# Kernel tuning notes

Hardware: AMD Instinct MI355X
Metric: run time of the kernel (lower is better)

## Reference

```python
import jax, jax.numpy as jnp
import numpy as np

K, D = 1024, 256


def setup_inputs() -> dict:
    key = jax.random.key(0)
    k1, k2 = jax.random.split(key)
    z_e = jax.random.normal(k1, (32, D, 32, 32), dtype=jnp.float32)
    # torch init: uniform_(-1/K, 1/K)
    emb_weight = jax.random.uniform(k2, (K, D), minval=-1.0 / K, maxval=1.0 / K, dtype=jnp.float32)
    return {"z_e": z_e, "emb_weight": emb_weight}


def reference(z_e, emb_weight):
    B, C, W, H = z_e.shape
    # [B, W, H, C] -> flatten to [N, C]
    z = jnp.transpose(z_e, (0, 2, 3, 1))
    z_flat = z.reshape(-1, C)
    # squared euclidean distances; argmin is identical to argmin of cdist
    d2 = (
        jnp.sum(z_flat * z_flat, axis=1, keepdims=True)
        - 2.0 * (z_flat @ emb_weight.T)
        + jnp.sum(emb_weight * emb_weight, axis=1)
    )  # [N, K]
    indices = jnp.argmin(d2, axis=1)  # [N]
    z_q = emb_weight[indices].reshape(B, W, H, C)
    # straight-through: forward value equals z_q, gradient passes to z_e
    z_q_st = z + jax.lax.stop_gradient(z_q - z)
    z_q_out = jnp.transpose(z_q, (0, 3, 1, 2))
    z_q_st_out = jnp.transpose(z_q_st, (0, 3, 1, 2))
    return (z_q_st_out, z_q_out, indices.reshape(B, W * H))
```

## Files before the change

### kernel.cpp

```cpp
#include <hip/hip_runtime.h>
#include <cfloat>
#include <cstdint>

#define THRESH 1.25e-4f

typedef __attribute__((ext_vector_type(8))) _Float16 half8;
typedef __attribute__((ext_vector_type(8))) unsigned short upk8;
typedef __attribute__((ext_vector_type(4))) float facc4;

__device__ __forceinline__ unsigned short f2h(float x) {
  _Float16 h = (_Float16)x;
  return __builtin_bit_cast(unsigned short, h);
}


__global__ __launch_bounds__(256) void precompute_kernel(
    const float* __restrict__ emb, float* __restrict__ Csq,
    unsigned short* __restrict__ ehT, int* __restrict__ flagCount) {
  int blk = blockIdx.x, t = threadIdx.x;
  if (blk < 4) {
    int k = blk * 256 + t;
    const float4* e4 = (const float4*)(emb + ((size_t)k << 8));
    double acc = 0.0;
    for (int d4 = 0; d4 < 64; ++d4) {
      float4 e = e4[d4];
      acc += (double)(e.x * e.x) + (double)(e.y * e.y) +
             (double)(e.z * e.z) + (double)(e.w * e.w);
    }
    Csq[k] = (float)acc;
    if (blk == 0 && t == 0) *flagCount = 0;
  } else {
    int linear = (blk - 4) * 256 + t;
    int code = linear & 1023, kg = linear >> 10;
    const float* ep = emb + ((size_t)code << 8) + (kg << 3);
    float4 e0 = *(const float4*)ep;
    float4 e1 = *(const float4*)(ep + 4);
    upk8 pk;
    pk[0] = f2h(e0.x); pk[1] = f2h(e0.y); pk[2] = f2h(e0.z); pk[3] = f2h(e0.w);
    pk[4] = f2h(e1.x); pk[5] = f2h(e1.y); pk[6] = f2h(e1.z); pk[7] = f2h(e1.w);
    *(upk8*)(ehT + ((size_t)linear << 3)) = pk;
  }
}

__device__ __forceinline__ void stage_slab(
    const unsigned short* __restrict__ ehT, char* slab, int s, int t) {
  int w6 = t & 0x1C0;
#pragma unroll
  for (int i = 0; i < 16; ++i) {
    int slot = (i << 9) + t;
    int kg = slot >> 8, cl = slot & 255;
    const unsigned short* g = ehT + (((size_t)(kg << 10) + (s << 8) + cl) << 3);
    char* lp = slab + (((i << 9) + w6) << 4);
    __builtin_amdgcn_global_load_lds(
        (const __attribute__((address_space(1))) unsigned int*)g,
        (__attribute__((address_space(3))) unsigned int*)lp, 16, 0, 0);
  }
}

__global__ __launch_bounds__(512, 2) void phase1_kernel(
    const float* __restrict__ z, const unsigned short* __restrict__ ehT,
    const float* __restrict__ Csq, float* __restrict__ A,
    int* __restrict__ idxbuf, int* __restrict__ flagCount,
    int* __restrict__ flagList) {
  __shared__ char slab[131072] __attribute__((aligned(16)));
  __shared__ float Cs[1024];
  __shared__ float mm1[2][4][32], mm2[2][4][32];
  __shared__ int mbi[2][4][32];

  int t = threadIdx.x;
  int n0 = blockIdx.x << 7;
  int b = n0 >> 10, wh0 = n0 & 1023;
  int w = t >> 6, l = t & 63;
  int wv = w & 3, wn = w >> 2;
  int lx = l & 15, lg = l >> 4;

  stage_slab(ehT, slab, 0, t);
  ((float2*)Cs)[t] = ((const float2*)Csq)[t];

  half8 afr[2][8];
  double nacc[2] = {0.0, 0.0};
  const float* zb = z + (((size_t)(b * 256)) << 10) + wh0 + wv * 32 + lx;
#pragma unroll
  for (int mi = 0; mi < 2; ++mi) {
#pragma unroll
    for (int kk = 0; kk < 8; ++kk) {
      upk8 pk;
#pragma unroll
      for (int j = 0; j < 8; ++j) {
        int c = kk * 32 + lg * 8 + j;
        float x = zb[((size_t)c << 10) + mi * 16];
        nacc[mi] += (double)(x * x);
        pk[j] = f2h(-2.0f * x);
      }
      afr[mi][kk] = __builtin_bit_cast(half8, pk);
    }
  }
#pragma unroll
  for (int mi = 0; mi < 2; ++mi) {
    double s = nacc[mi];
    s += __shfl_xor(s, 16);
    s += __shfl_xor(s, 32);
    if (wn == 0 && lg == 0) A[n0 + wv * 32 + mi * 16 + lx] = (float)s;
  }
  __syncthreads();

  float m1[8], m2[8];
  int bi[8];
#pragma unroll
  for (int s8 = 0; s8 < 8; ++s8) { m1[s8] = FLT_MAX; m2[s8] = FLT_MAX; bi[s8] = 0; }

  for (int s = 0; s < 4; ++s) {
    facc4 acc[2][8];
#pragma unroll
    for (int mi = 0; mi < 2; ++mi)
#pragma unroll
      for (int nj = 0; nj < 8; ++nj) {
        facc4 zf = {0.0f, 0.0f, 0.0f, 0.0f};
        acc[mi][nj] = zf;
      }
#pragma unroll
    for (int kk = 0; kk < 8; ++kk) {
      const char* base = slab + ((((kk << 2) + lg) << 8) + (wn << 7) + lx) * 16;
#pragma unroll
      for (int nj = 0; nj < 8; ++nj) {
        half8 bv = *(const half8*)(base + (nj << 8));
        acc[0][nj] = __builtin_amdgcn_mfma_f32_16x16x32_f16(afr[0][kk], bv, acc[0][nj], 0, 0, 0);
        acc[1][nj] = __builtin_amdgcn_mfma_f32_16x16x32_f16(afr[1][kk], bv, acc[1][nj], 0, 0, 0);
      }
    }
    int cbase = s * 256 + wn * 128;
#pragma unroll
    for (int nj = 0; nj < 8; ++nj) {
      float csv = Cs[cbase + nj * 16 + lx];
      int code = cbase + nj * 16 + lx;
#pragma unroll
      for (int mi = 0; mi < 2; ++mi)
#pragma unroll
        for (int reg = 0; reg < 4; ++reg) {
          int s8 = mi * 4 + reg;
          float sv = acc[mi][nj][reg] + csv;
          float hi = fmaxf(sv, m1[s8]);
          bool lt = sv < m1[s8];
          m1[s8] = lt ? sv : m1[s8];
          bi[s8] = lt ? code : bi[s8];
          m2[s8] = fminf(m2[s8], hi);
        }
    }
    __syncthreads();
    if (s < 3) {
      stage_slab(ehT, slab, s + 1, t);
      __syncthreads();
    }
  }

#pragma unroll
  for (int s8 = 0; s8 < 8; ++s8) {
    float M1 = m1[s8], M2 = m2[s8];
    int BI = bi[s8];
    for (int off = 8; off > 0; off >>= 1) {
      float om1 = __shfl_xor(M1, off, 16);
      float om2 = __shfl_xor(M2, off, 16);
      int obi = __shfl_xor(BI, off, 16);
      float lo = fminf(M2, om2);
      bool take = (om1 < M1) || (om1 == M1 && obi < BI);
      float loser = take ? M1 : om1;
      M2 = fminf(lo, loser);
      if (take) { M1 = om1; BI = obi; }
    }
    if (lx == 0) {
      int row = ((s8 >> 2) << 4) + (lg << 2) + (s8 & 3);
      mm1[wn][wv][row] = M1; mm2[wn][wv][row] = M2; mbi[wn][wv][row] = BI;
    }
  }
  __syncthreads();
  if (wn == 0 && lx == 0) {
#pragma unroll
    for (int s8 = 0; s8 < 8; ++s8) {
      int row = ((s8 >> 2) << 4) + (lg << 2) + (s8 & 3);
      float a1v = mm1[0][wv][row], a2v = mm2[0][wv][row];
      int ab = mbi[0][wv][row];
      float b1v = mm1[1][wv][row], b2v = mm2[1][wv][row];
      int bb = mbi[1][wv][row];
      bool tb = (b1v < a1v) || (b1v == a1v && bb < ab);
      float M1 = tb ? b1v : a1v;
      int BI = tb ? bb : ab;
      float M2 = fminf(fminf(a2v, b2v), tb ? a1v : b1v);
      int n = n0 + wv * 32 + row;
      idxbuf[n] = BI;
      if (M2 - M1 < THRESH) {
        int pos = atomicAdd(flagCount, 1);
        flagList[pos] = n;
      }
    }
  }
}

__global__ __launch_bounds__(256) void phase2_kernel(
    const float* __restrict__ z, const float* __restrict__ emb,
    const float* __restrict__ Csq, const float* __restrict__ A,
    int* __restrict__ idxbuf, const int* __restrict__ flagCount,
    const int* __restrict__ flagList) {
  __shared__ float zq[4][260];
  __shared__ float Anv[4];
  __shared__ int nn[4];
  __shared__ float sq[4][4];
  __shared__ int sk[4][4];
  int t = threadIdx.x;
  int w = t >> 6, l = t & 63;
  int cnt = *flagCount;
  int nit = (cnt + 3) >> 2;
  for (int it = blockIdx.x; it < nit; it += gridDim.x) {
    __syncthreads();
    int base = it << 2;
    int mcnt = min(4, cnt - base);
    if (t < 4) {
      if (t < mcnt) { int n = flagList[base + t]; nn[t] = n; Anv[t] = A[n]; }
      else nn[t] = -1;
    }
    __syncthreads();
#pragma unroll
    for (int v = 0; v < 4; ++v) {
      int n = nn[v];
      if (n >= 0) {
        int bb = n >> 10, wh = n & 1023;
        zq[v][t] = z[(((size_t)(bb * 256 + t)) << 10) + wh];
      }
    }
    __syncthreads();

    float dot[4][4];
#pragma unroll
    for (int r = 0; r < 4; ++r)
#pragma unroll
      for (int v = 0; v < 4; ++v) dot[r][v] = 0.0f;

    const float4* e0 = (const float4*)(emb + ((size_t)(t + 0) << 8));
    const float4* e1 = (const float4*)(emb + ((size_t)(t + 256) << 8));
    const float4* e2 = (const float4*)(emb + ((size_t)(t + 512) << 8));
    const float4* e3 = (const float4*)(emb + ((size_t)(t + 768) << 8));
#pragma unroll 8
    for (int d4 = 0; d4 < 64; ++d4) {
      float4 ea = e0[d4], eb = e1[d4], ec = e2[d4], ed = e3[d4];
#pragma unroll
      for (int v = 0; v < 4; ++v) {
        float4 zv = *(const float4*)&zq[v][d4 * 4];
        dot[0][v] += zv.x * ea.x + zv.y * ea.y + zv.z * ea.z + zv.w * ea.w;
        dot[1][v] += zv.x * eb.x + zv.y * eb.y + zv.z * eb.z + zv.w * eb.w;
        dot[2][v] += zv.x * ec.x + zv.y * ec.y + zv.z * ec.z + zv.w * ec.w;
        dot[3][v] += zv.x * ed.x + zv.y * ed.y + zv.z * ed.z + zv.w * ed.w;
      }
    }

    float bq[4];
    int bk[4];
#pragma unroll
    for (int v = 0; v < 4; ++v) { bq[v] = FLT_MAX; bk[v] = 0; }
#pragma unroll
    for (int r = 0; r < 4; ++r) {
      int k = t + (r << 8);
      float Ck = Csq[k];
#pragma unroll
      for (int v = 0; v < 4; ++v) {
        float qv = (Anv[v] - 2.0f * dot[r][v]) + Ck;
        if (qv < bq[v]) { bq[v] = qv; bk[v] = k; }
      }
    }

#pragma unroll
    for (int v = 0; v < 4; ++v) {
      float q = bq[v];
      int kk = bk[v];
      for (int off = 32; off > 0; off >>= 1) {
        float oq = __shfl_xor(q, off);
        int ok = __shfl_xor(kk, off);
        if (oq < q || (oq == q && ok < kk)) { q = oq; kk = ok; }
      }
      if (l == 0) { sq[v][w] = q; sk[v][w] = kk; }
    }
    __syncthreads();
    if (t < mcnt) {
      float q = sq[t][0];
      int kk = sk[t][0];
#pragma unroll
      for (int j = 1; j < 4; ++j) {
        float oq = sq[t][j];
        int ok = sk[t][j];
        if (oq < q || (oq == q && ok < kk)) { q = oq; kk = ok; }
      }
      idxbuf[nn[t]] = kk;
    }
  }
}

__global__ __launch_bounds__(256) void gather_kernel(
    const float* __restrict__ emb, const int* __restrict__ idxbuf,
    float* __restrict__ out) {
  __shared__ int sidx[32];
  __shared__ float se[256][34];
  int tid = threadIdx.x;
  int blk = blockIdx.x;
  int n0 = blk * 32;
  int b = n0 >> 10, wh0 = n0 & 1023;
  float* out0 = out;
  float* out1 = out + 8388608;
  float* out2 = out + 16777216;
  if (tid < 32) {
    int ix = idxbuf[n0 + tid];
    sidx[tid] = ix;
    out2[n0 + tid] = (float)ix;
  }
  __syncthreads();
  {
    int v = tid >> 3, d8 = tid & 7;
    int row = sidx[v];
    const float4* e4 = (const float4*)(emb + ((size_t)row << 8));
    for (int it = 0; it < 8; ++it) {
      int d4 = it * 8 + d8;
      float4 e = e4[d4];
      se[d4 * 4 + 0][v] = e.x; se[d4 * 4 + 1][v] = e.y;
      se[d4 * 4 + 2][v] = e.z; se[d4 * 4 + 3][v] = e.w;
    }
  }
  __syncthreads();
  {
    int v = tid & 31, cg = tid >> 5;
    for (int c = cg; c < 256; c += 8) {
      float val = se[c][v];
      size_t o = (((size_t)(b * 256 + c)) << 10) + wh0 + v;
      out0[o] = val;
      out1[o] = val;
    }
  }
}

extern "C" void kernel_launch(void* const* d_in, const int* in_sizes, int n_in,
                              void* d_out, int out_size, void* d_ws, size_t ws_size,
                              hipStream_t stream) {
  const float* z = (const float*)d_in[0];
  const float* emb = (const float*)d_in[1];
  float* ws = (float*)d_ws;
  float* Csq = ws;
  float* A = ws + 1024;
  int* idxbuf = (int*)(ws + 33792);
  int* flagCount = (int*)(ws + 66560);
  int* flagList = (int*)(ws + 66576);
  unsigned short* ehT = (unsigned short*)(ws + 99344);

  precompute_kernel<<<132, 256, 0, stream>>>(emb, Csq, ehT, flagCount);
  phase1_kernel<<<256, 512, 0, stream>>>(z, ehT, Csq, A, idxbuf, flagCount, flagList);
  phase2_kernel<<<1024, 256, 0, stream>>>(z, emb, Csq, A, idxbuf, flagCount, flagList);
  gather_kernel<<<1024, 256, 0, stream>>>(emb, idxbuf, (float*)d_out);
}
```

Before: 102.3 us.

## Double-buffer codebook LDS staging to overlap global loads with MFMA compute

Splits the 128KB codebook slab into two 64KB buffers of 128 codes each and walks the codebook in eight halves. The load for half h+2 is issued into the buffer just consumed, with vmcnt waits so that only the older batch must land before the next compute. This is meant to hide global-to-LDS staging latency behind MFMA work, which the old stage, sync, compute loop serialised. The cost is more barriers and smaller per-iteration tiles, and correctness now depends on the hand-written waitcnt and barrier sequence.

```diff
diff --git a/kernel.cpp b/kernel.cpp
--- a/kernel.cpp
+++ b/kernel.cpp
@@ -42,15 +42,15 @@
   }
 }
 
-__device__ __forceinline__ void stage_slab(
-    const unsigned short* __restrict__ ehT, char* slab, int s, int t) {
+__device__ __forceinline__ void stage_half(
+    const unsigned short* __restrict__ ehT, char* buf, int h, int t) {
   int w6 = t & 0x1C0;
 #pragma unroll
-  for (int i = 0; i < 16; ++i) {
+  for (int i = 0; i < 8; ++i) {
     int slot = (i << 9) + t;
-    int kg = slot >> 8, cl = slot & 255;
-    const unsigned short* g = ehT + (((size_t)(kg << 10) + (s << 8) + cl) << 3);
-    char* lp = slab + (((i << 9) + w6) << 4);
+    int kg = slot >> 7, cl = slot & 127;
+    const unsigned short* g = ehT + (((size_t)(kg << 10) + (h << 7) + cl) << 3);
+    char* lp = buf + (((i << 9) + w6) << 4);
     __builtin_amdgcn_global_load_lds(
         (const __attribute__((address_space(1))) unsigned int*)g,
         (__attribute__((address_space(3))) unsigned int*)lp, 16, 0, 0);
@@ -62,7 +62,8 @@
     const float* __restrict__ Csq, float* __restrict__ A,
     int* __restrict__ idxbuf, int* __restrict__ flagCount,
     int* __restrict__ flagList) {
-  __shared__ char slab[131072] __attribute__((aligned(16)));
+  __shared__ char bufA[65536] __attribute__((aligned(16)));
+  __shared__ char bufB[65536] __attribute__((aligned(16)));
   __shared__ float Cs[1024];
   __shared__ float mm1[2][4][32], mm2[2][4][32];
   __shared__ int mbi[2][4][32];
@@ -74,7 +75,8 @@
   int wv = w & 3, wn = w >> 2;
   int lx = l & 15, lg = l >> 4;
 
-  stage_slab(ehT, slab, 0, t);
+  stage_half(ehT, bufA, 0, t);
+  stage_half(ehT, bufB, 1, t);
   ((float2*)Cs)[t] = ((const float2*)Csq)[t];
 
   half8 afr[2][8];
@@ -109,28 +111,30 @@
 #pragma unroll
   for (int s8 = 0; s8 < 8; ++s8) { m1[s8] = FLT_MAX; m2[s8] = FLT_MAX; bi[s8] = 0; }
 
-  for (int s = 0; s < 4; ++s) {
-    facc4 acc[2][8];
+#pragma unroll
+  for (int h = 0; h < 8; ++h) {
+    const char* buf = (h & 1) ? bufB : bufA;
+    facc4 acc[2][4];
 #pragma unroll
     for (int mi = 0; mi < 2; ++mi)
 #pragma unroll
-      for (int nj = 0; nj < 8; ++nj) {
+      for (int nj = 0; nj < 4; ++nj) {
         facc4 zf = {0.0f, 0.0f, 0.0f, 0.0f};
         acc[mi][nj] = zf;
       }
 #pragma unroll
     for (int kk = 0; kk < 8; ++kk) {
-      const char* base = slab + ((((kk << 2) + lg) << 8) + (wn << 7) + lx) * 16;
-#pragma unroll
-      for (int nj = 0; nj < 8; ++nj) {
+      const char* base = buf + (((((kk << 2) + lg) << 7) + (wn << 6) + lx) << 4);
+#pragma unroll
+      for (int nj = 0; nj < 4; ++nj) {
         half8 bv = *(const half8*)(base + (nj << 8));
         acc[0][nj] = __builtin_amdgcn_mfma_f32_16x16x32_f16(afr[0][kk], bv, acc[0][nj], 0, 0, 0);
         acc[1][nj] = __builtin_amdgcn_mfma_f32_16x16x32_f16(afr[1][kk], bv, acc[1][nj], 0, 0, 0);
       }
     }
-    int cbase = s * 256 + wn * 128;
-#pragma unroll
-    for (int nj = 0; nj < 8; ++nj) {
+    int cbase = (h << 7) + (wn << 6);
+#pragma unroll
+    for (int nj = 0; nj < 4; ++nj) {
       float csv = Cs[cbase + nj * 16 + lx];
       int code = cbase + nj * 16 + lx;
 #pragma unroll
@@ -146,10 +150,16 @@
           m2[s8] = fminf(m2[s8], hi);
         }
     }
-    __syncthreads();
-    if (s < 3) {
-      stage_slab(ehT, slab, s + 1, t);
-      __syncthreads();
+    if (h < 7) {
+      asm volatile("s_waitcnt lgkmcnt(0)" ::: "memory");
+      __builtin_amdgcn_s_barrier();
+      if (h + 2 < 8) {
+        stage_half(ehT, (h & 1) ? bufB : bufA, h + 2, t);
+        asm volatile("s_waitcnt vmcnt(8)" ::: "memory");
+      } else {
+        asm volatile("s_waitcnt vmcnt(0)" ::: "memory");
+      }
+      __builtin_amdgcn_s_barrier();
     }
   }
 
```

Measured after the change: 124.3 us. 21.5% more time.

## Split distance GEMM into 128x128 tiled kernel with partial argmin merge

Applied to the files above, without the earlier changes.

Precompute now also transposes z into a row-major fp16 [N,256] buffer (stored in the output region) along with row norms. The fused phase1 kernel, which held a 128-point A fragment in registers and streamed the whole codebook through 128KB of LDS, is replaced by a conventional 128x128 tiled MFMA GEMM. It uses swizzled LDS staging, 2048 blocks and higher occupancy, and writes per-tile top-2 partials. A new merge kernel reduces the 8 code-tile partials and flags near-ties. The cost is extra kernel launches and global traffic for the fp16 z copy and the partial buffers.

```diff
diff --git a/kernel.cpp b/kernel.cpp
--- a/kernel.cpp
+++ b/kernel.cpp
@@ -13,11 +13,21 @@
   return __builtin_bit_cast(unsigned short, h);
 }
 
+__device__ __forceinline__ void glds16(const unsigned short* g, char* l) {
+  __builtin_amdgcn_global_load_lds(
+      (const __attribute__((address_space(1))) unsigned int*)g,
+      (__attribute__((address_space(3))) unsigned int*)l, 16, 0, 0);
+}
+
 
 __global__ __launch_bounds__(256) void precompute_kernel(
-    const float* __restrict__ emb, float* __restrict__ Csq,
-    unsigned short* __restrict__ ehT, int* __restrict__ flagCount) {
+    const float* __restrict__ z, const float* __restrict__ emb,
+    float* __restrict__ Csq, unsigned short* __restrict__ eh2,
+    unsigned short* __restrict__ zh2, float* __restrict__ A,
+    int* __restrict__ flagCount) {
   int blk = blockIdx.x, t = threadIdx.x;
+  __shared__ float zraw[128 * 66];
+  __shared__ double nrm[4][64];
   if (blk < 4) {
     int k = blk * 256 + t;
     const float4* e4 = (const float4*)(emb + ((size_t)k << 8));
@@ -29,132 +39,133 @@
     }
     Csq[k] = (float)acc;
     if (blk == 0 && t == 0) *flagCount = 0;
-  } else {
+  } else if (blk < 132) {
     int linear = (blk - 4) * 256 + t;
-    int code = linear & 1023, kg = linear >> 10;
-    const float* ep = emb + ((size_t)code << 8) + (kg << 3);
+    const float* ep = emb + ((size_t)linear << 3);
     float4 e0 = *(const float4*)ep;
     float4 e1 = *(const float4*)(ep + 4);
     upk8 pk;
     pk[0] = f2h(e0.x); pk[1] = f2h(e0.y); pk[2] = f2h(e0.z); pk[3] = f2h(e0.w);
     pk[4] = f2h(e1.x); pk[5] = f2h(e1.y); pk[6] = f2h(e1.z); pk[7] = f2h(e1.w);
-    *(upk8*)(ehT + ((size_t)linear << 3)) = pk;
-  }
-}
-
-__device__ __forceinline__ void stage_slab(
-    const unsigned short* __restrict__ ehT, char* slab, int s, int t) {
-  int w6 = t & 0x1C0;
-#pragma unroll
-  for (int i = 0; i < 16; ++i) {
-    int slot = (i << 9) + t;
-    int kg = slot >> 8, cl = slot & 255;
-    const unsigned short* g = ehT + (((size_t)(kg << 10) + (s << 8) + cl) << 3);
-    char* lp = slab + (((i << 9) + w6) << 4);
-    __builtin_amdgcn_global_load_lds(
-        (const __attribute__((address_space(1))) unsigned int*)g,
-        (__attribute__((address_space(3))) unsigned int*)lp, 16, 0, 0);
-  }
-}
-
-__global__ __launch_bounds__(512, 2) void phase1_kernel(
-    const float* __restrict__ z, const unsigned short* __restrict__ ehT,
-    const float* __restrict__ Csq, float* __restrict__ A,
-    int* __restrict__ idxbuf, int* __restrict__ flagCount,
-    int* __restrict__ flagList) {
-  __shared__ char slab[131072] __attribute__((aligned(16)));
-  __shared__ float Cs[1024];
-  __shared__ float mm1[2][4][32], mm2[2][4][32];
-  __shared__ int mbi[2][4][32];
+    *(upk8*)(eh2 + ((size_t)linear << 3)) = pk;
+  } else {
+    int zb = blk - 132;
+    int n0 = zb * 64;
+    int b = n0 >> 10, wh0 = n0 & 1023;
+    int v_l = t & 63, cg = t >> 6;
+    int part = t & 3, vv = t >> 2;
+    double nacc = 0.0;
+    for (int r = 0; r < 2; ++r) {
+      __syncthreads();
+      const float* zp = z + (((size_t)(b * 256 + r * 128 + cg * 32)) << 10) + wh0 + v_l;
+      for (int m = 0; m < 32; ++m) zraw[(cg * 32 + m) * 66 + v_l] = zp[(size_t)m << 10];
+      __syncthreads();
+#pragma unroll
+      for (int m = 0; m < 4; ++m) {
+        int c0 = part * 32 + m * 8;
+        upk8 pk;
+#pragma unroll
+        for (int j = 0; j < 8; ++j) {
+          float x = zraw[(c0 + j) * 66 + vv];
+          nacc += (double)(x * x);
+          pk[j] = f2h(-2.0f * x);
+        }
+        *(upk8*)(zh2 + (((size_t)(n0 + vv)) << 8) + r * 128 + c0) = pk;
+      }
+    }
+    nrm[part][vv] = nacc;
+    __syncthreads();
+    if (t < 64) A[n0 + t] = (float)(nrm[0][t] + nrm[1][t] + nrm[2][t] + nrm[3][t]);
+  }
+}
+
+__global__ __launch_bounds__(256, 4) void gemm_kernel(
+    const unsigned short* __restrict__ zh2, const unsigned short* __restrict__ eh2,
+    const float* __restrict__ Csq, float* __restrict__ pm1,
+    float* __restrict__ pm2, int* __restrict__ pbi) {
+  __shared__ char As[16384] __attribute__((aligned(16)));
+  __shared__ char Bs[16384] __attribute__((aligned(16)));
+  __shared__ float mm1[2][2][64], mm2[2][2][64];
+  __shared__ int mbi[2][2][64];
+  __shared__ float mer1[128], mer2[128];
+  __shared__ int meri[128];
 
   int t = threadIdx.x;
-  int n0 = blockIdx.x << 7;
-  int b = n0 >> 10, wh0 = n0 & 1023;
+  int bid = blockIdx.x;
+  int ntile = bid >> 8, mtile = bid & 255;
+  int n0 = mtile << 7, cb0 = ntile << 7;
   int w = t >> 6, l = t & 63;
-  int wv = w & 3, wn = w >> 2;
+  int wm = w & 1, wn = w >> 1;
   int lx = l & 15, lg = l >> 4;
 
-  stage_slab(ehT, slab, 0, t);
-  ((float2*)Cs)[t] = ((const float2*)Csq)[t];
-
-  half8 afr[2][8];
-  double nacc[2] = {0.0, 0.0};
-  const float* zb = z + (((size_t)(b * 256)) << 10) + wh0 + wv * 32 + lx;
-#pragma unroll
-  for (int mi = 0; mi < 2; ++mi) {
-#pragma unroll
-    for (int kk = 0; kk < 8; ++kk) {
-      upk8 pk;
-#pragma unroll
-      for (int j = 0; j < 8; ++j) {
-        int c = kk * 32 + lg * 8 + j;
-        float x = zb[((size_t)c << 10) + mi * 16];
-        nacc[mi] += (double)(x * x);
-        pk[j] = f2h(-2.0f * x);
-      }
-      afr[mi][kk] = __builtin_bit_cast(half8, pk);
-    }
-  }
-#pragma unroll
-  for (int mi = 0; mi < 2; ++mi) {
-    double s = nacc[mi];
-    s += __shfl_xor(s, 16);
-    s += __shfl_xor(s, 32);
-    if (wn == 0 && lg == 0) A[n0 + wv * 32 + mi * 16 + lx] = (float)s;
-  }
-  __syncthreads();
-
-  float m1[8], m2[8];
-  int bi[8];
-#pragma unroll
-  for (int s8 = 0; s8 < 8; ++s8) { m1[s8] = FLT_MAX; m2[s8] = FLT_MAX; bi[s8] = 0; }
-
-  for (int s = 0; s < 4; ++s) {
-    facc4 acc[2][8];
-#pragma unroll
-    for (int mi = 0; mi < 2; ++mi)
-#pragma unroll
-      for (int nj = 0; nj < 8; ++nj) {
-        facc4 zf = {0.0f, 0.0f, 0.0f, 0.0f};
-        acc[mi][nj] = zf;
-      }
-#pragma unroll
-    for (int kk = 0; kk < 8; ++kk) {
-      const char* base = slab + ((((kk << 2) + lg) << 8) + (wn << 7) + lx) * 16;
-#pragma unroll
-      for (int nj = 0; nj < 8; ++nj) {
-        half8 bv = *(const half8*)(base + (nj << 8));
-        acc[0][nj] = __builtin_amdgcn_mfma_f32_16x16x32_f16(afr[0][kk], bv, acc[0][nj], 0, 0, 0);
-        acc[1][nj] = __builtin_amdgcn_mfma_f32_16x16x32_f16(afr[1][kk], bv, acc[1][nj], 0, 0, 0);
-      }
-    }
-    int cbase = s * 256 + wn * 128;
-#pragma unroll
-    for (int nj = 0; nj < 8; ++nj) {
-      float csv = Cs[cbase + nj * 16 + lx];
-      int code = cbase + nj * 16 + lx;
-#pragma unroll
-      for (int mi = 0; mi < 2; ++mi)
-#pragma unroll
-        for (int reg = 0; reg < 4; ++reg) {
-          int s8 = mi * 4 + reg;
-          float sv = acc[mi][nj][reg] + csv;
-          float hi = fmaxf(sv, m1[s8]);
-          bool lt = sv < m1[s8];
-          m1[s8] = lt ? sv : m1[s8];
-          bi[s8] = lt ? code : bi[s8];
-          m2[s8] = fminf(m2[s8], hi);
-        }
-    }
-    __syncthreads();
-    if (s < 3) {
-      stage_slab(ehT, slab, s + 1, t);
-      __syncthreads();
-    }
-  }
-
-#pragma unroll
-  for (int s8 = 0; s8 < 8; ++s8) {
+  facc4 acc[4][4];
+#pragma unroll
+  for (int mi = 0; mi < 4; ++mi)
+#pragma unroll
+    for (int nj = 0; nj < 4; ++nj) {
+      facc4 zf = {0.0f, 0.0f, 0.0f, 0.0f};
+      acc[mi][nj] = zf;
+    }
+
+#pragma unroll 1
+  for (int kb = 0; kb < 256; kb += 64) {
+#pragma unroll
+    for (int i = 0; i < 4; ++i) {
+      int slot = (i << 8) + t;
+      int row = slot >> 3, craw = slot & 7;
+      int csrc = craw ^ (row & 7);
+      char* ldst = (char*)0 + (((i << 8) + (w << 6)) << 4);
+      glds16(zh2 + (((size_t)(n0 + row)) << 8) + kb + (csrc << 3), As + (size_t)ldst);
+      glds16(eh2 + (((size_t)(cb0 + row)) << 8) + kb + (csrc << 3), Bs + (size_t)ldst);
+    }
+    __syncthreads();
+#pragma unroll
+    for (int s = 0; s < 2; ++s) {
+      half8 a[4], bf[4];
+#pragma unroll
+      for (int mi = 0; mi < 4; ++mi) {
+        int row = wm * 64 + mi * 16 + lx;
+        int j = s * 4 + lg;
+        a[mi] = *(const half8*)(As + (((row << 3) + (j ^ (row & 7))) << 4));
+      }
+#pragma unroll
+      for (int nj = 0; nj < 4; ++nj) {
+        int row = wn * 64 + nj * 16 + lx;
+        int j = s * 4 + lg;
+        bf[nj] = *(const half8*)(Bs + (((row << 3) + (j ^ (row & 7))) << 4));
+      }
+#pragma unroll
+      for (int mi = 0; mi < 4; ++mi)
+#pragma unroll
+        for (int nj = 0; nj < 4; ++nj)
+          acc[mi][nj] = __builtin_amdgcn_mfma_f32_16x16x32_f16(a[mi], bf[nj], acc[mi][nj], 0, 0, 0);
+    }
+    __syncthreads();
+  }
+
+  float m1[16], m2[16];
+  int bi[16];
+#pragma unroll
+  for (int s8 = 0; s8 < 16; ++s8) { m1[s8] = FLT_MAX; m2[s8] = FLT_MAX; bi[s8] = 0; }
+#pragma unroll
+  for (int nj = 0; nj < 4; ++nj) {
+    int code = cb0 + wn * 64 + nj * 16 + lx;
+    float csv = Csq[code];
+#pragma unroll
+    for (int mi = 0; mi < 4; ++mi)
+#pragma unroll
+      for (int reg = 0; reg < 4; ++reg) {
+        int s8 = mi * 4 + reg;
+        float sv = acc[mi][nj][reg] + csv;
+        float hi = fmaxf(sv, m1[s8]);
+        bool lt = sv < m1[s8];
+        m1[s8] = lt ? sv : m1[s8];
+        bi[s8] = lt ? code : bi[s8];
+        m2[s8] = fminf(m2[s8], hi);
+      }
+  }
+#pragma unroll
+  for (int s8 = 0; s8 < 16; ++s8) {
     float M1 = m1[s8], M2 = m2[s8];
     int BI = bi[s8];
     for (int off = 8; off > 0; off >>= 1) {
@@ -169,29 +180,52 @@
     }
     if (lx == 0) {
       int row = ((s8 >> 2) << 4) + (lg << 2) + (s8 & 3);
-      mm1[wn][wv][row] = M1; mm2[wn][wv][row] = M2; mbi[wn][wv][row] = BI;
+      mm1[wn][wm][row] = M1; mm2[wn][wm][row] = M2; mbi[wn][wm][row] = BI;
     }
   }
   __syncthreads();
   if (wn == 0 && lx == 0) {
 #pragma unroll
-    for (int s8 = 0; s8 < 8; ++s8) {
+    for (int s8 = 0; s8 < 16; ++s8) {
       int row = ((s8 >> 2) << 4) + (lg << 2) + (s8 & 3);
-      float a1v = mm1[0][wv][row], a2v = mm2[0][wv][row];
-      int ab = mbi[0][wv][row];
-      float b1v = mm1[1][wv][row], b2v = mm2[1][wv][row];
-      int bb = mbi[1][wv][row];
+      float a1v = mm1[0][wm][row], a2v = mm2[0][wm][row];
+      int ab = mbi[0][wm][row];
+      float b1v = mm1[1][wm][row], b2v = mm2[1][wm][row];
+      int bb = mbi[1][wm][row];
       bool tb = (b1v < a1v) || (b1v == a1v && bb < ab);
       float M1 = tb ? b1v : a1v;
       int BI = tb ? bb : ab;
       float M2 = fminf(fminf(a2v, b2v), tb ? a1v : b1v);
-      int n = n0 + wv * 32 + row;
-      idxbuf[n] = BI;
-      if (M2 - M1 < THRESH) {
-        int pos = atomicAdd(flagCount, 1);
-        flagList[pos] = n;
-      }
-    }
+      mer1[wm * 64 + row] = M1; mer2[wm * 64 + row] = M2; meri[wm * 64 + row] = BI;
+    }
+  }
+  __syncthreads();
+  if (t < 128) {
+    size_t o = (size_t)ntile * 32768 + n0 + t;
+    pm1[o] = mer1[t]; pm2[o] = mer2[t]; pbi[o] = meri[t];
+  }
+}
+
+__global__ __launch_bounds__(256) void merge_kernel(
+    const float* __restrict__ pm1, const float* __restrict__ pm2,
+    const int* __restrict__ pbi, int* __restrict__ idxbuf,
+    int* __restrict__ flagCount, int* __restrict__ flagList) {
+  int n = blockIdx.x * 256 + threadIdx.x;
+  float M1 = pm1[n], M2 = pm2[n];
+  int BI = pbi[n];
+#pragma unroll
+  for (int j = 1; j < 8; ++j) {
+    float b1 = pm1[(size_t)j * 32768 + n], b2 = pm2[(size_t)j * 32768 + n];
+    int bb = pbi[(size_t)j * 32768 + n];
+    bool tb = (b1 < M1) || (b1 == M1 && bb < BI);
+    float loser = tb ? M1 : b1;
+    M2 = fminf(fminf(M2, b2), loser);
+    if (tb) { M1 = b1; BI = bb; }
+  }
+  idxbuf[n] = BI;
+  if (M2 - M1 < THRESH) {
+    int pos = atomicAdd(flagCount, 1);
+    flagList[pos] = n;
   }
 }
 
@@ -344,10 +378,16 @@
   int* idxbuf = (int*)(ws + 33792);
   int* flagCount = (int*)(ws + 66560);
   int* flagList = (int*)(ws + 66576);
-  unsigned short* ehT = (unsigned short*)(ws + 99344);
-
-  precompute_kernel<<<132, 256, 0, stream>>>(emb, Csq, ehT, flagCount);
-  phase1_kernel<<<256, 512, 0, stream>>>(z, ehT, Csq, A, idxbuf, flagCount, flagList);
+  unsigned short* eh2 = (unsigned short*)(ws + 99344);
+
+  unsigned short* zh2 = (unsigned short*)d_out;
+  float* pm1 = (float*)d_out + 4194304;
+  float* pm2 = pm1 + 262144;
+  int* pbi = (int*)(pm2 + 262144);
+
+  precompute_kernel<<<644, 256, 0, stream>>>(z, emb, Csq, eh2, zh2, A, flagCount);
+  gemm_kernel<<<2048, 256, 0, stream>>>(zh2, eh2, Csq, pm1, pm2, pbi);
+  merge_kernel<<<128, 256, 0, stream>>>(pm1, pm2, pbi, idxbuf, flagCount, flagList);
   phase2_kernel<<<1024, 256, 0, stream>>>(z, emb, Csq, A, idxbuf, flagCount, flagList);
   gather_kernel<<<1024, 256, 0, stream>>>(emb, idxbuf, (float*)d_out);
 }
```

After: 118.1 us. 15.4% more time.
